# Kernel optimization log

Measured on AMD Instinct MI355X. Metric: run time of the kernel, lower is better.

## Reference

```python
import jax, jax.numpy as jnp
import numpy as np

N, E, B, M = 50000, 100000, 50, 50
NPG = N // B            # atoms per graph
DIN, H1, H2, DE, AAF, G = 32, 32, 64, 16, 95, 128
K, T = 3, 6             # ARMA num_stacks, num_layers
F1, F2, F3 = 64, 32, 16
EA = 2 * (M - 1)        # amino-acid edges per graph


def setup_inputs() -> dict:
    key = jax.random.key(0)
    ks = jax.random.split(key, 24)
    s = 0.05
    def w(k, shape):
        return jax.random.normal(k, shape, jnp.float32) * s
    return {
        "x": jax.random.normal(ks[0], (N, DIN), jnp.float32),
        "edge_attr": jax.random.normal(ks[1], (E, DE), jnp.float32),
        "aa_features": jax.random.normal(ks[2], (B, M, AAF), jnp.float32),
        "edge_index": jax.random.randint(ks[3], (2, E), 0, N),
        "monomer_labels": jax.random.randint(ks[4], (B, NPG), 0, M),
        "amino_edge_index": jax.random.randint(ks[5], (2, EA), 0, M),
        "W_e1": w(ks[6], (DE, DIN * H1)), "b_e1": jnp.zeros((DIN * H1,), jnp.float32),
        "root1": w(ks[7], (DIN, H1)), "bias1": jnp.zeros((H1,), jnp.float32),
        "W_e2": w(ks[8], (DE, H1 * H2)), "b_e2": jnp.zeros((H1 * H2,), jnp.float32),
        "root2": w(ks[9], (H1, H2)), "bias2": jnp.zeros((H2,), jnp.float32),
        "Wa_atom": w(ks[10], (H2, 1)), "ba_atom": jnp.zeros((1,), jnp.float32),
        "arma_init_w": w(ks[11], (K, H2 + AAF, G)),
        "arma_w": w(ks[12], (T - 1, K, G, G)),
        "arma_root_w": w(ks[13], (T, K, H2 + AAF, G)),
        "arma_bias": jnp.zeros((T, K, G), jnp.float32),
        "Wa_aa": w(ks[14], (G, 1)), "ba_aa": jnp.zeros((1,), jnp.float32),
        "W1": w(ks[15], (G, F1)), "b1": jnp.zeros((F1,), jnp.float32),
        "W2": w(ks[16], (F1, F2)), "b2": jnp.zeros((F2,), jnp.float32),
        "W3": w(ks[17], (F2, F3)), "b3": jnp.zeros((F3,), jnp.float32),
        "W4": w(ks[18], (F3, 1)), "b4": jnp.zeros((1,), jnp.float32),
    }


def _nnconv(h, src, dst, edge_attr, Wm, bm, root, bias, fin, fout):
    # NNConv (aggr='add'): edge MLP -> per-edge weight matrix, gather-matmul-scatter
    w_e = (edge_attr @ Wm + bm).reshape(-1, fin, fout)            # [E, fin, fout]
    msg = jnp.einsum('ef,efo->eo', h[src], w_e)                   # [E, fout]
    agg = jax.ops.segment_sum(msg, dst, num_segments=h.shape[0])  # scatter-add to targets
    return agg + h @ root + bias


def _forward(x, edge_attr, aa_features, W_e1, b_e1, root1, bias1, W_e2, b_e2, root2, bias2,
             Wa_atom, ba_atom, arma_init_w, arma_w, arma_root_w, arma_bias, Wa_aa, ba_aa,
             W1, b1, W2, b2, W3, b3, W4, b4, edge_index, monomer_labels, amino_edge_index):
    src, dst = edge_index[0], edge_index[1]
    h = jax.nn.relu(_nnconv(x, src, dst, edge_attr, W_e1, b_e1, root1, bias1, DIN, H1))
    h = jax.nn.relu(_nnconv(h, src, dst, edge_attr, W_e2, b_e2, root2, bias2, H1, H2))

    # per-graph attention readout over atoms -> amino-acid embeddings (scatter by monomer label)
    xg = h.reshape(B, NPG, H2)
    attn = jax.nn.softmax(xg @ Wa_atom + ba_atom, axis=1)         # softmax over atoms in graph
    wx = xg * attn
    aa = jax.vmap(lambda wxi, lbl: jax.ops.segment_sum(wxi, lbl, num_segments=M))(wx, monomer_labels)
    h_aa = jnp.concatenate([aa, aa_features], axis=-1)            # [B, M, H2+95]

    # ARMAConv: gcn_norm without self-loops on amino-acid graph (shared across graphs)
    asrc, adst = amino_edge_index[0], amino_edge_index[1]
    deg = jax.ops.segment_sum(jnp.ones((EA,), x.dtype), adst, num_segments=M)
    dinv = jnp.where(deg > 0, 1.0 / jnp.sqrt(jnp.maximum(deg, 1.0)), 0.0)
    norm = dinv[asrc] * dinv[adst]                                # [EA]

    def arma(x0):  # x0: [M, H2+95]
        out = jnp.einsum('mf,kfo->kmo', x0, arma_init_w)          # [K, M, G]
        for t in range(T):
            if t > 0:
                out = jnp.einsum('kmo,kop->kmp', out, arma_w[t - 1])
            msg = out[:, asrc] * norm[None, :, None]              # [K, EA, G]
            prop = jax.vmap(lambda m: jax.ops.segment_sum(m, adst, num_segments=M))(msg)
            rootc = jnp.einsum('mf,kfo->kmo', x0, arma_root_w[t])
            out = jax.nn.relu(prop + rootc + arma_bias[t][:, None, :])
        return out.mean(axis=0)                                   # mean over stacks -> [M, G]

    g = jax.vmap(arma)(h_aa)                                      # [B, M, G]

    # attention readout over amino acids
    attn2 = jax.nn.softmax(g @ Wa_aa + ba_aa, axis=1)
    p = jnp.sum(g * attn2, axis=1)                                # [B, G]

    p = jax.nn.relu(p @ W1 + b1)
    p = jax.nn.relu(p @ W2 + b2)
    p = jax.nn.relu(p @ W3 + b3)
    p = p @ W4 + b4
    return p.reshape(-1)                                          # [B]


def reference(x, edge_attr, aa_features, edge_index, monomer_labels, amino_edge_index,
              W_e1, b_e1, root1, bias1, W_e2, b_e2, root2, bias2, Wa_atom, ba_atom,
              arma_init_w, arma_w, arma_root_w, arma_bias, Wa_aa, ba_aa,
              W1, b1, W2, b2, W3, b3, W4, b4):
    return _forward(x, edge_attr, aa_features, W_e1, b_e1, root1, bias1, W_e2, b_e2, root2, bias2,
                    Wa_atom, ba_atom, arma_init_w, arma_w, arma_root_w, arma_bias, Wa_aa, ba_aa,
                    W1, b1, W2, b2, W3, b3, W4, b4, edge_index, monomer_labels, amino_edge_index)
```

## Files before the change

kernel.cpp:

```cpp
#include <hip/hip_runtime.h>
#include <math.h>

#define N_ATOMS 50000
#define E_EDGES 100000
#define B_G     50
#define M_M     50
#define NPG     1000
#define DIN     32
#define H1C     32
#define H2C     64
#define DEC     16
#define AAF     95
#define G_DIM   128
#define K_ST    3
#define T_L     6
#define EA_E    98
#define XDIM    159
#define NS      21
#define MPAD    64
#define GP      132
#define KP2     168
#define KW      544
#define SLC     10
#define APB     100
#define NSB     ((N_ATOMS + 255) / 256)

typedef __attribute__((ext_vector_type(8))) short bf16x8;
typedef __attribute__((ext_vector_type(4))) float f32x4;
typedef __attribute__((ext_vector_type(4))) unsigned int u32x4;

__device__ __forceinline__ short f2bf(float f) {
    unsigned int u = __float_as_uint(f);
    unsigned int r = (u + 0x7FFFu + ((u >> 16) & 1u)) >> 16;
    return (short)r;
}
__device__ __forceinline__ float bf2f(short b) {
    return __uint_as_float(((unsigned int)(unsigned short)b) << 16);
}
__device__ __forceinline__ unsigned int cvtpk_bf16(float lo, float hi) {
    unsigned int r;
    asm("v_cvt_pk_bf16_f32 %0, %1, %2" : "=v"(r) : "v"(lo), "v"(hi));
    return r;
}

__device__ __forceinline__ void f4fma(float4& d, float s, const float4& v) {
    d.x += s * v.x; d.y += s * v.y; d.z += s * v.z; d.w += s * v.w;
}
__device__ __forceinline__ void f4add(float4& d, const float4& v) {
    d.x += v.x; d.y += v.y; d.z += v.z; d.w += v.w;
}
__device__ __forceinline__ void f4relu(float4& d) {
    d.x = fmaxf(d.x, 0.f); d.y = fmaxf(d.y, 0.f);
    d.z = fmaxf(d.z, 0.f); d.w = fmaxf(d.w, 0.f);
}

__global__ __launch_bounds__(256) void deg_count(const int* __restrict__ eidx,
                                                 int* __restrict__ deg)
{
    int e = blockIdx.x * 256 + threadIdx.x;
    if (e >= E_EDGES) return;
    atomicAdd(&deg[eidx[E_EDGES + e]], 1);
}

__global__ __launch_bounds__(256) void scan_part(const int* __restrict__ deg,
                                                 int* __restrict__ bsum)
{
    __shared__ int tmp[256];
    int tid = threadIdx.x;
    int n = blockIdx.x * 256 + tid;
    tmp[tid] = (n < N_ATOMS) ? deg[n] : 0;
    __syncthreads();
    for (int off = 128; off > 0; off >>= 1) {
        if (tid < off) tmp[tid] += tmp[tid + off];
        __syncthreads();
    }
    if (tid == 0) bsum[blockIdx.x] = tmp[0];
}

__global__ __launch_bounds__(256) void scan_mid(const int* __restrict__ bsum,
                                                int* __restrict__ bpre)
{
    __shared__ int tmp[256];
    int tid = threadIdx.x;
    int v = (tid < NSB) ? bsum[tid] : 0;
    tmp[tid] = v;
    __syncthreads();
    for (int off = 1; off < 256; off <<= 1) {
        int t = tmp[tid];
        int add = (tid >= off) ? tmp[tid - off] : 0;
        __syncthreads();
        tmp[tid] = t + add;
        __syncthreads();
    }
    if (tid < NSB) bpre[tid] = tmp[tid] - v;
}

__global__ __launch_bounds__(256) void scan_out(int* __restrict__ deg_off,
                                                const int* __restrict__ bpre)
{
    __shared__ int tmp[256];
    int tid = threadIdx.x;
    int n = blockIdx.x * 256 + tid;
    int v = (n < N_ATOMS) ? deg_off[n] : 0;
    tmp[tid] = v;
    __syncthreads();
    for (int off = 1; off < 256; off <<= 1) {
        int t = tmp[tid];
        int add = (tid >= off) ? tmp[tid - off] : 0;
        __syncthreads();
        tmp[tid] = t + add;
        __syncthreads();
    }
    int incl = tmp[tid];
    int base = bpre[blockIdx.x];
    if (n < N_ATOMS) deg_off[n] = base + incl - v;
    if (n == N_ATOMS - 1) deg_off[N_ATOMS] = base + incl;
}

__global__ __launch_bounds__(256) void fill_order(const int* __restrict__ eidx,
                                                  const int* __restrict__ off,
                                                  int* __restrict__ cursor,
                                                  int* __restrict__ order)
{
    int e = blockIdx.x * 256 + threadIdx.x;
    if (e >= E_EDGES) return;
    int d = eidx[E_EDGES + e];
    int pos = atomicAdd(&cursor[d], 1);
    order[off[d] + pos] = e;
}

template<int FOUT>
__global__ __launch_bounds__(256) void prep_we(
    const float* __restrict__ We, const float* __restrict__ be,
    short* __restrict__ WB)
{
    int idx = blockIdx.x * 256 + threadIdx.x;
    if (idx >= FOUT * KW) return;
    int o = idx / KW, k = idx - o * KW;
    float v = (k < 512) ? We[(size_t)k * FOUT + o]
                        : be[(size_t)(k - 512) * FOUT + o];
    WB[(size_t)o * KW + k] = f2bf(v);
}

template<int FOUT, int NTT, int WGRP, int MTB>
__global__ __launch_bounds__(256) void edge_msg_v2(
    const float* __restrict__ h, const float* __restrict__ ea,
    const int* __restrict__ eidx, const short* __restrict__ WB,
    float* __restrict__ msg)
{
    constexpr int KS = 17;
    int tid  = threadIdx.x;
    int lane = tid & 63, wave = tid >> 6;
    int l16  = lane & 15, quad = lane >> 4;
    int nt   = wave % NTT, tg = wave / NTT;
    int ebase = blockIdx.x * (MTB * 16);

    bf16x8 Bfr[KS];
    {
        const short* wb = WB + (size_t)(nt * 16 + l16) * KW;
        #pragma unroll
        for (int ks = 0; ks < KS; ++ks)
            Bfr[ks] = *(const bf16x8*)(wb + ks * 32 + quad * 8);
    }

    for (int t = tg; t < MTB; t += WGRP) {
        int e  = ebase + t * 16 + l16;
        int es = (e < E_EDGES) ? e : (E_EDGES - 1);
        int s  = eidx[es];
        float4 h0 = *(const float4*)(h + (size_t)s * 32 + quad * 8);
        float4 h1 = *(const float4*)(h + (size_t)s * 32 + quad * 8 + 4);
        float hf[8] = {h0.x, h0.y, h0.z, h0.w, h1.x, h1.y, h1.z, h1.w};
        float4 e0 = *(const float4*)(ea + (size_t)es * DEC);
        float4 e1 = *(const float4*)(ea + (size_t)es * DEC + 4);
        float4 e2 = *(const float4*)(ea + (size_t)es * DEC + 8);
        float4 e3 = *(const float4*)(ea + (size_t)es * DEC + 12);
        float eaf[16] = {e0.x, e0.y, e0.z, e0.w, e1.x, e1.y, e1.z, e1.w,
                         e2.x, e2.y, e2.z, e2.w, e3.x, e3.y, e3.z, e3.w};

        f32x4 acc = (f32x4){0.f, 0.f, 0.f, 0.f};
        #pragma unroll
        for (int ks = 0; ks < KS; ++ks) {
            u32x4 av;
            if (ks < DEC) {
                float fac = eaf[ks];
                #pragma unroll
                for (int j = 0; j < 4; ++j)
                    av[j] = cvtpk_bf16(fac * hf[2 * j], fac * hf[2 * j + 1]);
            } else {
                #pragma unroll
                for (int j = 0; j < 4; ++j)
                    av[j] = cvtpk_bf16(hf[2 * j], hf[2 * j + 1]);
            }
            bf16x8 a = __builtin_bit_cast(bf16x8, av);
            acc = __builtin_amdgcn_mfma_f32_16x16x32_bf16(a, Bfr[ks], acc, 0, 0, 0);
        }
        int erb = ebase + t * 16 + quad * 4;
        float* mp = msg + (size_t)erb * FOUT + nt * 16 + l16;
        #pragma unroll
        for (int r = 0; r < 4; ++r) {
            if (erb + r < E_EDGES) mp[(size_t)r * FOUT] = acc[r];
        }
    }
}

template<int FIN, int FOUT>
__global__ __launch_bounds__(256) void gather_update(
    const float* __restrict__ msg, const int* __restrict__ off,
    const int* __restrict__ order, const float* __restrict__ hin,
    const float* __restrict__ root, const float* __restrict__ bias,
    float* __restrict__ hout)
{
    constexpr int NPB = 256 / FOUT;
    __shared__ float rlds[FIN][FOUT];
    __shared__ float hlds[NPB][FIN];
    int tid = threadIdx.x;
    for (int i = tid; i < FIN * FOUT / 4; i += 256) {
        *(float4*)&rlds[0][i * 4] = *(const float4*)(root + i * 4);
    }
    int nb = blockIdx.x * NPB;
    for (int i = tid; i < NPB * FIN; i += 256) {
        int ln = i / FIN, f = i % FIN;
        int n = nb + ln;
        hlds[ln][f] = (n < N_ATOMS) ? hin[(size_t)n * FIN + f] : 0.f;
    }
    __syncthreads();

    int ln = tid / FOUT, o = tid % FOUT;
    int n = nb + ln;
    if (n >= N_ATOMS) return;
    float acc = bias[o];
    #pragma unroll 8
    for (int f = 0; f < FIN; ++f) acc += hlds[ln][f] * rlds[f][o];
    int j0 = off[n], j1 = off[n + 1];
    for (int j = j0; j < j1; ++j) {
        int e = order[j];
        acc += msg[(size_t)e * FOUT + o];
    }
    hout[(size_t)n * FOUT + o] = fmaxf(acc, 0.f);
}

__global__ __launch_bounds__(256) void atom_score(
    const float* __restrict__ h2, const float* __restrict__ wa,
    const float* __restrict__ ba, float* __restrict__ sc)
{
    __shared__ float hl[128][65];
    int nb = blockIdx.x * 128;
    int tid = threadIdx.x;
    for (int i = tid; i < 128 * 16; i += 256) {
        int r = i >> 4, c4 = i & 15;
        int n = nb + r;
        float4 v = (n < N_ATOMS) ? *(const float4*)(h2 + (size_t)n * H2C + c4 * 4)
                                 : make_float4(0.f, 0.f, 0.f, 0.f);
        *(float4*)&hl[r][c4 * 4] = v;
    }
    __syncthreads();
    if (tid < 128) {
        int n = nb + tid;
        if (n < N_ATOMS) {
            float sv = ba[0];
            #pragma unroll 8
            for (int o = 0; o < H2C; ++o) sv += hl[tid][o] * wa[o];
            sc[n] = sv;
        }
    }
}

__global__ __launch_bounds__(256) void graph_softmax(float* __restrict__ sc)
{
    __shared__ float red[256];
    int b = blockIdx.x, tid = threadIdx.x;
    float* sb = sc + (size_t)b * NPG;
    float lmax = -1e30f;
    for (int n = tid; n < NPG; n += 256) lmax = fmaxf(lmax, sb[n]);
    red[tid] = lmax;
    __syncthreads();
    for (int off = 128; off > 0; off >>= 1) {
        if (tid < off) red[tid] = fmaxf(red[tid], red[tid + off]);
        __syncthreads();
    }
    float mx = red[0];
    __syncthreads();
    float lsum = 0.f;
    for (int n = tid; n < NPG; n += 256) lsum += expf(sb[n] - mx);
    red[tid] = lsum;
    __syncthreads();
    for (int off = 128; off > 0; off >>= 1) {
        if (tid < off) red[tid] += red[tid + off];
        __syncthreads();
    }
    float inv = 1.f / red[0];
    __syncthreads();
    for (int n = tid; n < NPG; n += 256) sb[n] = expf(sb[n] - mx) * inv;
}

__global__ __launch_bounds__(256) void atom_scatter(
    const float* __restrict__ h2, const float* __restrict__ wn,
    const int* __restrict__ labels, float* __restrict__ partial)
{
    __shared__ float aa4[4][M_M][H2C];
    int b = blockIdx.x / SLC, s = blockIdx.x % SLC;
    int tid = threadIdx.x;
    int wave = tid >> 6, lane = tid & 63;
    for (int i = tid; i < 4 * M_M * H2C; i += 256) ((float*)aa4)[i] = 0.f;
    __syncthreads();
    int nbase = s * APB;
    const float* hb = h2 + (size_t)b * NPG * H2C;
    #pragma unroll 5
    for (int it = 0; it < APB / 4; ++it) {
        int n = nbase + it * 4 + wave;
        int lbl = labels[b * NPG + n];
        float w = wn[(size_t)b * NPG + n];
        float hv = hb[(size_t)n * H2C + lane];
        aa4[wave][lbl][lane] += hv * w;
    }
    __syncthreads();
    float* pb = partial + (size_t)(b * SLC + s) * M_M * H2C;
    for (int i = tid; i < M_M * H2C; i += 256) {
        float v = ((float*)aa4)[i] + ((float*)aa4)[M_M * H2C + i]
                + ((float*)aa4)[2 * M_M * H2C + i] + ((float*)aa4)[3 * M_M * H2C + i];
        pb[i] = v;
    }
}

__global__ __launch_bounds__(256) void x0_finalize(
    const float* __restrict__ partial, const float* __restrict__ aaf,
    short* __restrict__ x0b)
{
    int idx = blockIdx.x * 256 + threadIdx.x;
    if (idx >= B_G * MPAD * KP2) return;
    int b = idx / (MPAD * KP2);
    int rem = idx - b * (MPAD * KP2);
    int m = rem / KP2, k = rem - m * KP2;
    float v = 0.f;
    if (m < M_M) {
        if (k < H2C) {
            const float* pb = partial + (size_t)b * SLC * M_M * H2C + m * H2C + k;
            #pragma unroll
            for (int s = 0; s < SLC; ++s) v += pb[(size_t)s * (M_M * H2C)];
        } else if (k < XDIM) {
            v = aaf[((size_t)b * M_M + m) * AAF + (k - H2C)];
        }
    }
    x0b[idx] = f2bf(v);
}

__global__ void aa_norm_kernel(const int* __restrict__ aei,
                               int* __restrict__ aa_off,
                               int* __restrict__ aa_src,
                               float* __restrict__ aa_nrm)
{
    __shared__ int   sdeg[M_M];
    __shared__ int   scur[M_M];
    __shared__ float sdinv[M_M];
    __shared__ int   soff[M_M + 1];
    int tid = threadIdx.x;
    if (tid < M_M) { sdeg[tid] = 0; scur[tid] = 0; }
    __syncthreads();
    if (tid < EA_E) atomicAdd(&sdeg[aei[EA_E + tid]], 1);
    __syncthreads();
    if (tid < M_M) {
        float dv = (float)sdeg[tid];
        sdinv[tid] = (dv > 0.f) ? (1.f / sqrtf(fmaxf(dv, 1.f))) : 0.f;
    }
    __syncthreads();
    if (tid == 0) {
        soff[0] = 0;
        for (int m = 0; m < M_M; ++m) soff[m + 1] = soff[m] + sdeg[m];
    }
    __syncthreads();
    if (tid < EA_E) {
        int ss = aei[tid], dd = aei[EA_E + tid];
        int pos = atomicAdd(&scur[dd], 1);
        int idx = soff[dd] + pos;
        aa_src[idx] = ss;
        aa_nrm[idx] = sdinv[ss] * sdinv[dd];
    }
    if (tid < M_M + 1) aa_off[tid] = soff[tid];
}

__global__ __launch_bounds__(256) void prep_wt(
    const float* __restrict__ init_w, const float* __restrict__ root_w,
    short* __restrict__ Wtb)
{
    int idx = blockIdx.x * 256 + threadIdx.x;
    if (idx >= NS * XDIM * G_DIM) return;
    int s = idx / (XDIM * G_DIM);
    int rem = idx - s * XDIM * G_DIM;
    int k = rem / G_DIM, n = rem - k * G_DIM;
    float v = (s < K_ST) ? init_w[idx]
                         : root_w[(size_t)(s - K_ST) * XDIM * G_DIM + rem];
    Wtb[(size_t)s * G_DIM * KP2 + n * KP2 + k] = f2bf(v);
}

__global__ __launch_bounds__(256) void prep_aw(
    const float* __restrict__ arma_w, short* __restrict__ Wab)
{
    int idx = blockIdx.x * 256 + threadIdx.x;
    if (idx >= (T_L - 1) * K_ST * G_DIM * G_DIM) return;
    int slot = idx / (G_DIM * G_DIM);
    int rem = idx - slot * G_DIM * G_DIM;
    int p = rem / G_DIM, n = rem - p * G_DIM;
    Wab[(size_t)slot * G_DIM * G_DIM + n * G_DIM + p] = f2bf(arma_w[idx]);
}

__global__ __launch_bounds__(256) void rc_gemm_mfma(
    const short* __restrict__ x0b, const short* __restrict__ Wtb,
    float* __restrict__ RC)
{
    int b = blockIdx.x / NS, s = blockIdx.x % NS;
    int tid = threadIdx.x;
    int lane = tid & 63, wave = tid >> 6;
    int l16 = lane & 15, quad = lane >> 4;
    const short* xa = x0b + (size_t)b * MPAD * KP2 + (wave * 16 + l16) * KP2;
    const short* wb = Wtb + (size_t)s * G_DIM * KP2;

    f32x4 acc[8];
    #pragma unroll
    for (int nt = 0; nt < 8; ++nt) acc[nt] = (f32x4){0.f, 0.f, 0.f, 0.f};

    #pragma unroll
    for (int ks = 0; ks < 5; ++ks) {
        bf16x8 a = *(const bf16x8*)(xa + ks * 32 + quad * 8);
        #pragma unroll
        for (int nt = 0; nt < 8; ++nt) {
            bf16x8 bf = *(const bf16x8*)(wb + (nt * 16 + l16) * KP2 + ks * 32 + quad * 8);
            acc[nt] = __builtin_amdgcn_mfma_f32_16x16x32_bf16(a, bf, acc[nt], 0, 0, 0);
        }
    }
    float* op = RC + (size_t)(b * NS + s) * M_M * G_DIM;
    #pragma unroll
    for (int nt = 0; nt < 8; ++nt) {
        #pragma unroll
        for (int r = 0; r < 4; ++r) {
            int m = wave * 16 + quad * 4 + r;
            if (m < M_M)
                op[m * G_DIM + nt * 16 + l16] = acc[nt][r];
        }
    }
}

__global__ __launch_bounds__(512) void arma_iter(
    const float* __restrict__ RC, const short* __restrict__ Wab,
    const float* __restrict__ arma_bias,
    const int* __restrict__ aa_off, const int* __restrict__ aa_src,
    const float* __restrict__ aa_nrm, float* __restrict__ gfull)
{
    __shared__ float Abuf[MPAD][GP];
    __shared__ float Bbuf[MPAD][GP];
    __shared__ int   s_off[M_M + 1];
    __shared__ int   s_src[EA_E];
    __shared__ float s_nrm[EA_E];
    int b = blockIdx.x / K_ST, k = blockIdx.x % K_ST;
    int tid = threadIdx.x;
    int oi = tid & 15, mi = tid >> 4;
    int c0 = oi * 4, c1 = 64 + oi * 4;
    int lane = tid & 63, wave = tid >> 6;
    int l16 = lane & 15, quad = lane >> 4;
    int mt = wave >> 1, nh = wave & 1;

    const float* rcb = RC + (size_t)b * NS * M_M * G_DIM;
    if (tid < M_M + 1) s_off[tid] = aa_off[tid];
    if (tid < EA_E) { s_src[tid] = aa_src[tid]; s_nrm[tid] = aa_nrm[tid]; }

    for (int i = tid; i < MPAD * G_DIM; i += 512) {
        int m = i >> 7, o = i & 127;
        Abuf[m][o] = (m < M_M) ? rcb[(size_t)k * M_M * G_DIM + i] : 0.f;
        Bbuf[m][o] = 0.f;
    }
    __syncthreads();

    for (int t = 0; t < T_L; ++t) {
        if (t > 0) {
            const short* aw = Wab + (size_t)((t - 1) * K_ST + k) * G_DIM * G_DIM;
            f32x4 acc[4];
            #pragma unroll
            for (int nt = 0; nt < 4; ++nt) acc[nt] = (f32x4){0.f, 0.f, 0.f, 0.f};
            #pragma unroll
            for (int ks = 0; ks < 4; ++ks) {
                bf16x8 a;
                const float* ap = &Bbuf[mt * 16 + l16][ks * 32 + quad * 8];
                #pragma unroll
                for (int j = 0; j < 8; ++j) a[j] = f2bf(ap[j]);
                #pragma unroll
                for (int nt = 0; nt < 4; ++nt) {
                    int n0 = (nh * 4 + nt) * 16 + l16;
                    bf16x8 bf = *(const bf16x8*)(aw + n0 * G_DIM + ks * 32 + quad * 8);
                    acc[nt] = __builtin_amdgcn_mfma_f32_16x16x32_bf16(a, bf, acc[nt], 0, 0, 0);
                }
            }
            #pragma unroll
            for (int nt = 0; nt < 4; ++nt) {
                #pragma unroll
                for (int r = 0; r < 4; ++r) {
                    Abuf[mt * 16 + quad * 4 + r][(nh * 4 + nt) * 16 + l16] = acc[nt][r];
                }
            }
            __syncthreads();
        }
        const float* rct = rcb + (size_t)(K_ST + t * K_ST + k) * M_M * G_DIM;
        const float* bb  = arma_bias + ((size_t)t * K_ST + k) * G_DIM;
        float4 bias0 = *(const float4*)(bb + c0);
        float4 bias1 = *(const float4*)(bb + c1);
        #pragma unroll
        for (int r = 0; r < 2; ++r) {
            int m = mi * 2 + r;
            if (m < M_M) {
                const float* rr = rct + (size_t)m * G_DIM;
                float4 v0 = bias0, v1 = bias1;
                f4add(v0, *(const float4*)(rr + c0));
                f4add(v1, *(const float4*)(rr + c1));
                int j0 = s_off[m], j1 = s_off[m + 1];
                for (int j = j0; j < j1; ++j) {
                    float nv = s_nrm[j];
                    const float* ap = &Abuf[s_src[j]][0];
                    f4fma(v0, nv, *(const float4*)(ap + c0));
                    f4fma(v1, nv, *(const float4*)(ap + c1));
                }
                f4relu(v0);
                f4relu(v1);
                *(float4*)&Bbuf[m][c0] = v0;
                *(float4*)&Bbuf[m][c1] = v1;
            }
        }
        __syncthreads();
    }
    float* gb = gfull + ((size_t)(b * K_ST + k)) * M_M * G_DIM;
    for (int i = tid; i < M_M * G_DIM; i += 512) {
        int m = i >> 7, o = i & 127;
        gb[i] = Bbuf[m][o];
    }
}

__global__ __launch_bounds__(128) void aa_readout_mlp(
    const float* __restrict__ gfull, const float* __restrict__ wa,
    const float* __restrict__ ba,
    const float* __restrict__ W1, const float* __restrict__ b1,
    const float* __restrict__ W2, const float* __restrict__ b2,
    const float* __restrict__ W3, const float* __restrict__ b3,
    const float* __restrict__ W4, const float* __restrict__ b4,
    float* __restrict__ out)
{
    __shared__ float g[M_M][G_DIM + 1];
    __shared__ float s2[M_M];
    __shared__ float p[G_DIM];
    __shared__ float r1[64], r2[32], r3[16];
    int b = blockIdx.x, tid = threadIdx.x;
    const float* g0 = gfull + (size_t)b * K_ST * M_M * G_DIM;
    for (int i = tid; i < M_M * G_DIM; i += 128) {
        int m = i >> 7, o = i & 127;
        g[m][o] = (g0[i] + g0[M_M*G_DIM + i] + g0[2*M_M*G_DIM + i]) * (1.f/3.f);
    }
    __syncthreads();
    if (tid < M_M) {
        float sv = ba[0];
        for (int o = 0; o < G_DIM; ++o) sv += g[tid][o] * wa[o];
        s2[tid] = sv;
    }
    __syncthreads();
    if (tid == 0) {
        float mx = -1e30f;
        for (int m = 0; m < M_M; ++m) mx = fmaxf(mx, s2[m]);
        float den = 0.f;
        for (int m = 0; m < M_M; ++m) den += expf(s2[m] - mx);
        float inv = 1.f / den;
        for (int m = 0; m < M_M; ++m) s2[m] = expf(s2[m] - mx) * inv;
    }
    __syncthreads();
    {
        float pv = 0.f;
        for (int m = 0; m < M_M; ++m) pv += g[m][tid] * s2[m];
        p[tid] = pv;
    }
    __syncthreads();
    if (tid < 64) {
        float v = b1[tid];
        for (int i = 0; i < 128; ++i) v += p[i] * W1[i * 64 + tid];
        r1[tid] = fmaxf(v, 0.f);
    }
    __syncthreads();
    if (tid < 32) {
        float v = b2[tid];
        for (int i = 0; i < 64; ++i) v += r1[i] * W2[i * 32 + tid];
        r2[tid] = fmaxf(v, 0.f);
    }
    __syncthreads();
    if (tid < 16) {
        float v = b3[tid];
        for (int i = 0; i < 32; ++i) v += r2[i] * W3[i * 16 + tid];
        r3[tid] = fmaxf(v, 0.f);
    }
    __syncthreads();
    if (tid == 0) {
        float v = b4[0];
        for (int i = 0; i < 16; ++i) v += r3[i] * W4[i];
        out[b] = v;
    }
}

extern "C" void kernel_launch(void* const* d_in, const int* in_sizes, int n_in,
                              void* d_out, int out_size, void* d_ws, size_t ws_size,
                              hipStream_t stream)
{
    (void)in_sizes; (void)n_in; (void)out_size; (void)ws_size;
    const float* x            = (const float*)d_in[0];
    const float* edge_attr    = (const float*)d_in[1];
    const float* aa_features  = (const float*)d_in[2];
    const int*   edge_index   = (const int*)  d_in[3];
    const int*   mono_labels  = (const int*)  d_in[4];
    const int*   amino_ei     = (const int*)  d_in[5];
    const float* W_e1 = (const float*)d_in[6];
    const float* b_e1 = (const float*)d_in[7];
    const float* root1= (const float*)d_in[8];
    const float* bias1= (const float*)d_in[9];
    const float* W_e2 = (const float*)d_in[10];
    const float* b_e2 = (const float*)d_in[11];
    const float* root2= (const float*)d_in[12];
    const float* bias2= (const float*)d_in[13];
    const float* Wa_atom = (const float*)d_in[14];
    const float* ba_atom = (const float*)d_in[15];
    const float* arma_init_w = (const float*)d_in[16];
    const float* arma_w      = (const float*)d_in[17];
    const float* arma_root_w = (const float*)d_in[18];
    const float* arma_bias   = (const float*)d_in[19];
    const float* Wa_aa = (const float*)d_in[20];
    const float* ba_aa = (const float*)d_in[21];
    const float* W1 = (const float*)d_in[22];
    const float* b1 = (const float*)d_in[23];
    const float* W2 = (const float*)d_in[24];
    const float* b2 = (const float*)d_in[25];
    const float* W3 = (const float*)d_in[26];
    const float* b3 = (const float*)d_in[27];
    const float* W4 = (const float*)d_in[28];
    const float* b4 = (const float*)d_in[29];

    float* ws = (float*)d_ws;
    float* h1    = ws;
    float* h2    = h1   + (size_t)N_ATOMS * H1C;
    float* h_aa  = h2   + (size_t)N_ATOMS * H2C;
    float* sc    = h_aa + (size_t)B_G * M_M * XDIM;
    int*   aa_off = (int*)(sc + (size_t)B_G * NPG);
    int*   aa_src = aa_off + (M_M + 1);
    float* aa_nrm = (float*)(aa_src + EA_E);
    int*   deg_off = (int*)(aa_nrm + EA_E);
    int*   cursor  = deg_off + (N_ATOMS + 1);
    int*   order   = cursor + N_ATOMS;
    int*   bsum    = order + E_EDGES;
    int*   bpre    = bsum + 256;
    float* RC    = (float*)(bpre + 256);
    float* gfull = RC + (size_t)B_G * NS * M_M * G_DIM;
    short* Wtb   = (short*)((((uintptr_t)(gfull + (size_t)B_G * K_ST * M_M * G_DIM)) + 15)
                            & ~(uintptr_t)15);
    short* x0b   = Wtb + (size_t)NS * G_DIM * KP2;
    short* Wab   = x0b + (size_t)B_G * MPAD * KP2;
    short* WB1   = Wab + (size_t)(T_L - 1) * K_ST * G_DIM * G_DIM;
    short* WB2   = WB1 + (size_t)H1C * KW;
    float* msg   = RC;
    float* partial = RC;
    (void)h_aa;

    (void)hipMemsetAsync(deg_off, 0, (2 * N_ATOMS + 1) * sizeof(int), stream);

    int eblocks = (E_EDGES + 255) / 256;

    deg_count<<<eblocks, 256, 0, stream>>>(edge_index, deg_off);
    scan_part<<<NSB, 256, 0, stream>>>(deg_off, bsum);
    scan_mid<<<1, 256, 0, stream>>>(bsum, bpre);
    scan_out<<<NSB, 256, 0, stream>>>(deg_off, bpre);
    fill_order<<<eblocks, 256, 0, stream>>>(edge_index, deg_off, cursor, order);

    prep_we<H1C><<<(H1C * KW + 255) / 256, 256, 0, stream>>>(W_e1, b_e1, WB1);
    prep_we<H2C><<<(H2C * KW + 255) / 256, 256, 0, stream>>>(W_e2, b_e2, WB2);
    prep_wt<<<(NS * XDIM * G_DIM + 255) / 256, 256, 0, stream>>>(
        arma_init_w, arma_root_w, Wtb);
    prep_aw<<<((T_L - 1) * K_ST * G_DIM * G_DIM + 255) / 256, 256, 0, stream>>>(
        arma_w, Wab);

    edge_msg_v2<H1C, 2, 2, 8><<<(E_EDGES + 127) / 128, 256, 0, stream>>>(
        x, edge_attr, edge_index, WB1, msg);
    gather_update<DIN, H1C><<<(N_ATOMS + 7) / 8, 256, 0, stream>>>(
        msg, deg_off, order, x, root1, bias1, h1);
    edge_msg_v2<H2C, 4, 1, 4><<<(E_EDGES + 63) / 64, 256, 0, stream>>>(
        h1, edge_attr, edge_index, WB2, msg);
    gather_update<H1C, H2C><<<(N_ATOMS + 3) / 4, 256, 0, stream>>>(
        msg, deg_off, order, h1, root2, bias2, h2);

    atom_score<<<(N_ATOMS + 127) / 128, 256, 0, stream>>>(h2, Wa_atom, ba_atom, sc);
    graph_softmax<<<B_G, 256, 0, stream>>>(sc);
    atom_scatter<<<B_G * SLC, 256, 0, stream>>>(h2, sc, mono_labels, partial);
    x0_finalize<<<(B_G * MPAD * KP2 + 255) / 256, 256, 0, stream>>>(
        partial, aa_features, x0b);

    aa_norm_kernel<<<1, 128, 0, stream>>>(amino_ei, aa_off, aa_src, aa_nrm);
    rc_gemm_mfma<<<B_G * NS, 256, 0, stream>>>(x0b, Wtb, RC);
    arma_iter<<<B_G * K_ST, 512, 0, stream>>>(RC, Wab, arma_bias,
                                              aa_off, aa_src, aa_nrm, gfull);
    aa_readout_mlp<<<B_G, 128, 0, stream>>>(gfull, Wa_aa, ba_aa, W1, b1, W2, b2, W3, b3, W4, b4,
                                            (float*)d_out);
}
```

Measured before the change: 336.7 us.

## Fuse prep kernels, scatter messages into CSR order, fuse atom scoring and softmax

```diff
diff --git a/kernel.cpp b/kernel.cpp
--- a/kernel.cpp
+++ b/kernel.cpp
@@ -25,6 +25,12 @@
 #define APB     100
 #define NSB     ((N_ATOMS + 255) / 256)
 
+#define OFF_WE2 (H1C * KW)
+#define OFF_WT  (OFF_WE2 + H2C * KW)
+#define OFF_AW  (OFF_WT + NS * XDIM * G_DIM)
+#define OFF_DEG (OFF_AW + (T_L - 1) * K_ST * G_DIM * G_DIM)
+#define PREP_TOTAL (OFF_DEG + E_EDGES)
+
 typedef __attribute__((ext_vector_type(8))) short bf16x8;
 typedef __attribute__((ext_vector_type(4))) float f32x4;
 typedef __attribute__((ext_vector_type(4))) unsigned int u32x4;
@@ -54,12 +60,75 @@
     d.z = fmaxf(d.z, 0.f); d.w = fmaxf(d.w, 0.f);
 }
 
-__global__ __launch_bounds__(256) void deg_count(const int* __restrict__ eidx,
-                                                 int* __restrict__ deg)
-{
-    int e = blockIdx.x * 256 + threadIdx.x;
-    if (e >= E_EDGES) return;
-    atomicAdd(&deg[eidx[E_EDGES + e]], 1);
+__global__ __launch_bounds__(256) void prep_all(
+    const float* __restrict__ We1, const float* __restrict__ be1, short* __restrict__ WB1,
+    const float* __restrict__ We2, const float* __restrict__ be2, short* __restrict__ WB2,
+    const float* __restrict__ init_w, const float* __restrict__ root_w, short* __restrict__ Wtb,
+    const float* __restrict__ arma_w, short* __restrict__ Wab,
+    const int* __restrict__ eidx, int* __restrict__ deg,
+    const int* __restrict__ aei, int* __restrict__ aa_off,
+    int* __restrict__ aa_src, float* __restrict__ aa_nrm)
+{
+    int tid = threadIdx.x;
+    if (blockIdx.x == 0) {
+        __shared__ int   sdeg[M_M];
+        __shared__ int   scur[M_M];
+        __shared__ float sdinv[M_M];
+        __shared__ int   soff[M_M + 1];
+        if (tid < M_M) { sdeg[tid] = 0; scur[tid] = 0; }
+        __syncthreads();
+        if (tid < EA_E) atomicAdd(&sdeg[aei[EA_E + tid]], 1);
+        __syncthreads();
+        if (tid < M_M) {
+            float dv = (float)sdeg[tid];
+            sdinv[tid] = (dv > 0.f) ? (1.f / sqrtf(fmaxf(dv, 1.f))) : 0.f;
+        }
+        __syncthreads();
+        if (tid == 0) {
+            soff[0] = 0;
+            for (int m = 0; m < M_M; ++m) soff[m + 1] = soff[m] + sdeg[m];
+        }
+        __syncthreads();
+        if (tid < EA_E) {
+            int ss = aei[tid], dd = aei[EA_E + tid];
+            int pos = atomicAdd(&scur[dd], 1);
+            int idx = soff[dd] + pos;
+            aa_src[idx] = ss;
+            aa_nrm[idx] = sdinv[ss] * sdinv[dd];
+        }
+        if (tid < M_M + 1) aa_off[tid] = soff[tid];
+        return;
+    }
+    int idx = (blockIdx.x - 1) * 256 + tid;
+    if (idx < OFF_WE2) {
+        int o = idx / KW, k = idx - o * KW;
+        float v = (k < 512) ? We1[(size_t)k * H1C + o]
+                            : be1[(size_t)(k - 512) * H1C + o];
+        WB1[idx] = f2bf(v);
+    } else if (idx < OFF_WT) {
+        int rem = idx - OFF_WE2;
+        int o = rem / KW, k = rem - o * KW;
+        float v = (k < 512) ? We2[(size_t)k * H2C + o]
+                            : be2[(size_t)(k - 512) * H2C + o];
+        WB2[rem] = f2bf(v);
+    } else if (idx < OFF_AW) {
+        int rem = idx - OFF_WT;
+        int s = rem / (XDIM * G_DIM);
+        int r2 = rem - s * XDIM * G_DIM;
+        int k = r2 / G_DIM, n = r2 - k * G_DIM;
+        float v = (s < K_ST) ? init_w[rem]
+                             : root_w[(size_t)(s - K_ST) * XDIM * G_DIM + r2];
+        Wtb[(size_t)s * G_DIM * KP2 + n * KP2 + k] = f2bf(v);
+    } else if (idx < OFF_DEG) {
+        int rem = idx - OFF_AW;
+        int slot = rem / (G_DIM * G_DIM);
+        int r2 = rem - slot * G_DIM * G_DIM;
+        int p = r2 / G_DIM, n = r2 - p * G_DIM;
+        Wab[(size_t)slot * G_DIM * G_DIM + n * G_DIM + p] = f2bf(arma_w[rem]);
+    } else if (idx < PREP_TOTAL) {
+        int e = idx - OFF_DEG;
+        atomicAdd(&deg[eidx[E_EDGES + e]], 1);
+    }
 }
 
 __global__ __launch_bounds__(256) void scan_part(const int* __restrict__ deg,
@@ -117,36 +186,23 @@
     if (n == N_ATOMS - 1) deg_off[N_ATOMS] = base + incl;
 }
 
-__global__ __launch_bounds__(256) void fill_order(const int* __restrict__ eidx,
-                                                  const int* __restrict__ off,
-                                                  int* __restrict__ cursor,
-                                                  int* __restrict__ order)
+__global__ __launch_bounds__(256) void fill_inv(const int* __restrict__ eidx,
+                                                const int* __restrict__ off,
+                                                int* __restrict__ cursor,
+                                                int* __restrict__ ipos)
 {
     int e = blockIdx.x * 256 + threadIdx.x;
     if (e >= E_EDGES) return;
     int d = eidx[E_EDGES + e];
     int pos = atomicAdd(&cursor[d], 1);
-    order[off[d] + pos] = e;
-}
-
-template<int FOUT>
-__global__ __launch_bounds__(256) void prep_we(
-    const float* __restrict__ We, const float* __restrict__ be,
-    short* __restrict__ WB)
-{
-    int idx = blockIdx.x * 256 + threadIdx.x;
-    if (idx >= FOUT * KW) return;
-    int o = idx / KW, k = idx - o * KW;
-    float v = (k < 512) ? We[(size_t)k * FOUT + o]
-                        : be[(size_t)(k - 512) * FOUT + o];
-    WB[(size_t)o * KW + k] = f2bf(v);
+    ipos[e] = off[d] + pos;
 }
 
 template<int FOUT, int NTT, int WGRP, int MTB>
 __global__ __launch_bounds__(256) void edge_msg_v2(
     const float* __restrict__ h, const float* __restrict__ ea,
-    const int* __restrict__ eidx, const short* __restrict__ WB,
-    float* __restrict__ msg)
+    const int* __restrict__ eidx, const int* __restrict__ ipos,
+    const short* __restrict__ WB, float* __restrict__ msg)
 {
     constexpr int KS = 17;
     int tid  = threadIdx.x;
@@ -195,20 +251,25 @@
             acc = __builtin_amdgcn_mfma_f32_16x16x32_bf16(a, Bfr[ks], acc, 0, 0, 0);
         }
         int erb = ebase + t * 16 + quad * 4;
-        float* mp = msg + (size_t)erb * FOUT + nt * 16 + l16;
         #pragma unroll
         for (int r = 0; r < 4; ++r) {
-            if (erb + r < E_EDGES) mp[(size_t)r * FOUT] = acc[r];
-        }
-    }
-}
-
-template<int FIN, int FOUT>
+            int ee = erb + r;
+            if (ee < E_EDGES) {
+                int p = ipos[ee];
+                msg[(size_t)p * FOUT + nt * 16 + l16] = acc[r];
+            }
+        }
+    }
+}
+
+template<int FIN, int FOUT, bool SCORE>
 __global__ __launch_bounds__(256) void gather_update(
     const float* __restrict__ msg, const int* __restrict__ off,
-    const int* __restrict__ order, const float* __restrict__ hin,
+    const float* __restrict__ hin,
     const float* __restrict__ root, const float* __restrict__ bias,
-    float* __restrict__ hout)
+    float* __restrict__ hout,
+    const float* __restrict__ wa, const float* __restrict__ ba,
+    float* __restrict__ sc)
 {
     constexpr int NPB = 256 / FOUT;
     __shared__ float rlds[FIN][FOUT];
@@ -233,43 +294,32 @@
     for (int f = 0; f < FIN; ++f) acc += hlds[ln][f] * rlds[f][o];
     int j0 = off[n], j1 = off[n + 1];
     for (int j = j0; j < j1; ++j) {
-        int e = order[j];
-        acc += msg[(size_t)e * FOUT + o];
-    }
-    hout[(size_t)n * FOUT + o] = fmaxf(acc, 0.f);
-}
-
-__global__ __launch_bounds__(256) void atom_score(
-    const float* __restrict__ h2, const float* __restrict__ wa,
-    const float* __restrict__ ba, float* __restrict__ sc)
-{
-    __shared__ float hl[128][65];
-    int nb = blockIdx.x * 128;
-    int tid = threadIdx.x;
-    for (int i = tid; i < 128 * 16; i += 256) {
-        int r = i >> 4, c4 = i & 15;
-        int n = nb + r;
-        float4 v = (n < N_ATOMS) ? *(const float4*)(h2 + (size_t)n * H2C + c4 * 4)
-                                 : make_float4(0.f, 0.f, 0.f, 0.f);
-        *(float4*)&hl[r][c4 * 4] = v;
-    }
-    __syncthreads();
-    if (tid < 128) {
-        int n = nb + tid;
-        if (n < N_ATOMS) {
-            float sv = ba[0];
-            #pragma unroll 8
-            for (int o = 0; o < H2C; ++o) sv += hl[tid][o] * wa[o];
-            sc[n] = sv;
-        }
-    }
-}
-
-__global__ __launch_bounds__(256) void graph_softmax(float* __restrict__ sc)
-{
+        acc += msg[(size_t)j * FOUT + o];
+    }
+    float hv = fmaxf(acc, 0.f);
+    hout[(size_t)n * FOUT + o] = hv;
+    if constexpr (SCORE) {
+        static_assert(FOUT == 64, "score fusion needs node==wave");
+        float sv = hv * wa[o];
+        #pragma unroll
+        for (int d = 32; d > 0; d >>= 1) sv += __shfl_down(sv, d);
+        if (o == 0) sc[n] = sv + ba[0];
+    }
+}
+
+__global__ __launch_bounds__(256) void atom_scatter_sm(
+    const float* __restrict__ h2, const float* __restrict__ sc,
+    const int* __restrict__ labels, float* __restrict__ partial)
+{
+    __shared__ float aa4[4][M_M][H2C];
     __shared__ float red[256];
-    int b = blockIdx.x, tid = threadIdx.x;
-    float* sb = sc + (size_t)b * NPG;
+    int b = blockIdx.x / SLC, s = blockIdx.x % SLC;
+    int tid = threadIdx.x;
+    int wave = tid >> 6, lane = tid & 63;
+    const float* sb = sc + (size_t)b * NPG;
+
+    for (int i = tid; i < 4 * M_M * H2C; i += 256) ((float*)aa4)[i] = 0.f;
+
     float lmax = -1e30f;
     for (int n = tid; n < NPG; n += 256) lmax = fmaxf(lmax, sb[n]);
     red[tid] = lmax;
@@ -290,26 +340,14 @@
     }
     float inv = 1.f / red[0];
     __syncthreads();
-    for (int n = tid; n < NPG; n += 256) sb[n] = expf(sb[n] - mx) * inv;
-}
-
-__global__ __launch_bounds__(256) void atom_scatter(
-    const float* __restrict__ h2, const float* __restrict__ wn,
-    const int* __restrict__ labels, float* __restrict__ partial)
-{
-    __shared__ float aa4[4][M_M][H2C];
-    int b = blockIdx.x / SLC, s = blockIdx.x % SLC;
-    int tid = threadIdx.x;
-    int wave = tid >> 6, lane = tid & 63;
-    for (int i = tid; i < 4 * M_M * H2C; i += 256) ((float*)aa4)[i] = 0.f;
-    __syncthreads();
+
     int nbase = s * APB;
     const float* hb = h2 + (size_t)b * NPG * H2C;
     #pragma unroll 5
     for (int it = 0; it < APB / 4; ++it) {
         int n = nbase + it * 4 + wave;
         int lbl = labels[b * NPG + n];
-        float w = wn[(size_t)b * NPG + n];
+        float w = expf(sb[n] - mx) * inv;
         float hv = hb[(size_t)n * H2C + lane];
         aa4[wave][lbl][lane] += hv * w;
     }
@@ -342,65 +380,6 @@
         }
     }
     x0b[idx] = f2bf(v);
-}
-
-__global__ void aa_norm_kernel(const int* __restrict__ aei,
-                               int* __restrict__ aa_off,
-                               int* __restrict__ aa_src,
-                               float* __restrict__ aa_nrm)
-{
-    __shared__ int   sdeg[M_M];
-    __shared__ int   scur[M_M];
-    __shared__ float sdinv[M_M];
-    __shared__ int   soff[M_M + 1];
-    int tid = threadIdx.x;
-    if (tid < M_M) { sdeg[tid] = 0; scur[tid] = 0; }
-    __syncthreads();
-    if (tid < EA_E) atomicAdd(&sdeg[aei[EA_E + tid]], 1);
-    __syncthreads();
-    if (tid < M_M) {
-        float dv = (float)sdeg[tid];
-        sdinv[tid] = (dv > 0.f) ? (1.f / sqrtf(fmaxf(dv, 1.f))) : 0.f;
-    }
-    __syncthreads();
-    if (tid == 0) {
-        soff[0] = 0;
-        for (int m = 0; m < M_M; ++m) soff[m + 1] = soff[m] + sdeg[m];
-    }
-    __syncthreads();
-    if (tid < EA_E) {
-        int ss = aei[tid], dd = aei[EA_E + tid];
-        int pos = atomicAdd(&scur[dd], 1);
-        int idx = soff[dd] + pos;
-        aa_src[idx] = ss;
-        aa_nrm[idx] = sdinv[ss] * sdinv[dd];
-    }
-    if (tid < M_M + 1) aa_off[tid] = soff[tid];
-}
-
-__global__ __launch_bounds__(256) void prep_wt(
-    const float* __restrict__ init_w, const float* __restrict__ root_w,
-    short* __restrict__ Wtb)
-{
-    int idx = blockIdx.x * 256 + threadIdx.x;
-    if (idx >= NS * XDIM * G_DIM) return;
-    int s = idx / (XDIM * G_DIM);
-    int rem = idx - s * XDIM * G_DIM;
-    int k = rem / G_DIM, n = rem - k * G_DIM;
-    float v = (s < K_ST) ? init_w[idx]
-                         : root_w[(size_t)(s - K_ST) * XDIM * G_DIM + rem];
-    Wtb[(size_t)s * G_DIM * KP2 + n * KP2 + k] = f2bf(v);
-}
-
-__global__ __launch_bounds__(256) void prep_aw(
-    const float* __restrict__ arma_w, short* __restrict__ Wab)
-{
-    int idx = blockIdx.x * 256 + threadIdx.x;
-    if (idx >= (T_L - 1) * K_ST * G_DIM * G_DIM) return;
-    int slot = idx / (G_DIM * G_DIM);
-    int rem = idx - slot * G_DIM * G_DIM;
-    int p = rem / G_DIM, n = rem - p * G_DIM;
-    Wab[(size_t)slot * G_DIM * G_DIM + n * G_DIM + p] = f2bf(arma_w[idx]);
 }
 
 __global__ __launch_bounds__(256) void rc_gemm_mfma(
@@ -643,8 +622,8 @@
     float* aa_nrm = (float*)(aa_src + EA_E);
     int*   deg_off = (int*)(aa_nrm + EA_E);
     int*   cursor  = deg_off + (N_ATOMS + 1);
-    int*   order   = cursor + N_ATOMS;
-    int*   bsum    = order + E_EDGES;
+    int*   ipos    = cursor + N_ATOMS;
+    int*   bsum    = ipos + E_EDGES;
     int*   bpre    = bsum + 256;
     float* RC    = (float*)(bpre + 256);
     float* gfull = RC + (size_t)B_G * NS * M_M * G_DIM;
@@ -662,35 +641,29 @@
 
     int eblocks = (E_EDGES + 255) / 256;
 
-    deg_count<<<eblocks, 256, 0, stream>>>(edge_index, deg_off);
+    prep_all<<<1 + (PREP_TOTAL + 255) / 256, 256, 0, stream>>>(
+        W_e1, b_e1, WB1, W_e2, b_e2, WB2,
+        arma_init_w, arma_root_w, Wtb, arma_w, Wab,
+        edge_index, deg_off, amino_ei, aa_off, aa_src, aa_nrm);
+
     scan_part<<<NSB, 256, 0, stream>>>(deg_off, bsum);
     scan_mid<<<1, 256, 0, stream>>>(bsum, bpre);
     scan_out<<<NSB, 256, 0, stream>>>(deg_off, bpre);
-    fill_order<<<eblocks, 256, 0, stream>>>(edge_index, deg_off, cursor, order);
-
-    prep_we<H1C><<<(H1C * KW + 255) / 256, 256, 0, stream>>>(W_e1, b_e1, WB1);
-    prep_we<H2C><<<(H2C * KW + 255) / 256, 256, 0, stream>>>(W_e2, b_e2, WB2);
-    prep_wt<<<(NS * XDIM * G_DIM + 255) / 256, 256, 0, stream>>>(
-        arma_init_w, arma_root_w, Wtb);
-    prep_aw<<<((T_L - 1) * K_ST * G_DIM * G_DIM + 255) / 256, 256, 0, stream>>>(
-        arma_w, Wab);
+    fill_inv<<<eblocks, 256, 0, stream>>>(edge_index, deg_off, cursor, ipos);
 
     edge_msg_v2<H1C, 2, 2, 8><<<(E_EDGES + 127) / 128, 256, 0, stream>>>(
-        x, edge_attr, edge_index, WB1, msg);
-    gather_update<DIN, H1C><<<(N_ATOMS + 7) / 8, 256, 0, stream>>>(
-        msg, deg_off, order, x, root1, bias1, h1);
+        x, edge_attr, edge_index, ipos, WB1, msg);
+    gather_update<DIN, H1C, false><<<(N_ATOMS + 7) / 8, 256, 0, stream>>>(
+        msg, deg_off, x, root1, bias1, h1, nullptr, nullptr, nullptr);
     edge_msg_v2<H2C, 4, 1, 4><<<(E_EDGES + 63) / 64, 256, 0, stream>>>(
-        h1, edge_attr, edge_index, WB2, msg);
-    gather_update<H1C, H2C><<<(N_ATOMS + 3) / 4, 256, 0, stream>>>(
-        msg, deg_off, order, h1, root2, bias2, h2);
-
-    atom_score<<<(N_ATOMS + 127) / 128, 256, 0, stream>>>(h2, Wa_atom, ba_atom, sc);
-    graph_softmax<<<B_G, 256, 0, stream>>>(sc);
-    atom_scatter<<<B_G * SLC, 256, 0, stream>>>(h2, sc, mono_labels, partial);
+        h1, edge_attr, edge_index, ipos, WB2, msg);
+    gather_update<H1C, H2C, true><<<(N_ATOMS + 3) / 4, 256, 0, stream>>>(
+        msg, deg_off, h1, root2, bias2, h2, Wa_atom, ba_atom, sc);
+
+    atom_scatter_sm<<<B_G * SLC, 256, 0, stream>>>(h2, sc, mono_labels, partial);
     x0_finalize<<<(B_G * MPAD * KP2 + 255) / 256, 256, 0, stream>>>(
         partial, aa_features, x0b);
 
-    aa_norm_kernel<<<1, 128, 0, stream>>>(amino_ei, aa_off, aa_src, aa_nrm);
     rc_gemm_mfma<<<B_G * NS, 256, 0, stream>>>(x0b, Wtb, RC);
     arma_iter<<<B_G * K_ST, 512, 0, stream>>>(RC, Wab, arma_bias,
                                               aa_off, aa_src, aa_nrm, gfull);
```

Result: faster. 318.0 us (-5.6%).
